# Performance work log

Hardware: AMD Instinct MI355X
Metric: run time of the kernel (lower is better)

The kernel has to match this reference:

```python
import jax, jax.numpy as jnp
import numpy as np

NUM_PERTS = 20000
D = 256          # embedding_dim
B, C = 64, 512   # batch_size, num_cells
EPS = 1e-5


def setup_inputs() -> dict:
    key = jax.random.key(0)
    ks = jax.random.split(key, 20)
    inp = {
        'perturbation_ids': jax.random.randint(ks[0], (B, C), 0, NUM_PERTS),
        'table': jax.random.normal(ks[1], (NUM_PERTS, D), dtype=jnp.float32),
    }
    s = 1.0 / np.sqrt(D)
    for i in range(4):
        inp[f'W{i+1}'] = jax.random.uniform(ks[2 + 2 * i], (D, D), minval=-s, maxval=s, dtype=jnp.float32)
        inp[f'b{i+1}'] = jax.random.uniform(ks[3 + 2 * i], (D,), minval=-s, maxval=s, dtype=jnp.float32)
    for i in range(3):
        inp[f'g{i+1}'] = jnp.ones((D,), jnp.float32)
        inp[f'be{i+1}'] = jnp.zeros((D,), jnp.float32)
    return inp


def _bn(x, gamma, beta):
    # BatchNorm1d forward with batch statistics (training-mode math, biased var)
    mu = jnp.mean(x, axis=0)
    var = jnp.mean(jnp.square(x - mu), axis=0)
    return (x - mu) * jax.lax.rsqrt(var + EPS) * gamma + beta


def reference(perturbation_ids, table,
              W1, b1, W2, b2, W3, b3, W4, b4,
              g1, be1, g2, be2, g3, be3):
    # Vectorized replacement of the Python double-loop dict gather
    emb = table[perturbation_ids]                 # (B, C, D)
    x = emb.reshape(-1, D)                        # (B*C, D)
    x = _bn(jax.nn.gelu(x @ W1 + b1, approximate=False), g1, be1)
    x = _bn(jax.nn.gelu(x @ W2 + b2, approximate=False), g2, be2)
    x = _bn(jax.nn.gelu(x @ W3 + b3, approximate=False), g3, be3)
    x = jax.nn.gelu(x @ W4 + b4, approximate=False)
    return x.reshape(B, C, D)
```

## Files before the change

### kernel.cpp

```cpp
#include <hip/hip_runtime.h>
#include <math.h>


typedef __attribute__((ext_vector_type(8))) short short8;
typedef __attribute__((ext_vector_type(4))) float floatx4;

#define DDIM 256

__device__ __forceinline__ unsigned short f2bf(float f) {
    union { float f; unsigned int u; } v; v.f = f;
    unsigned int r = v.u + 0x7fffu + ((v.u >> 16) & 1u);
    return (unsigned short)(r >> 16);
}
__device__ __forceinline__ float bf2f(unsigned short u) {
    union { unsigned int i; float f; } v; v.i = ((unsigned int)u) << 16;
    return v.f;
}
__device__ __forceinline__ float gelu_fast(float x) {
    float z = 0.7978845608f * (x + 0.044715f * x * x * x);
    float e = __expf(2.0f * z);
    float th = 1.0f - 2.0f * __builtin_amdgcn_rcpf(1.0f + e);
    return 0.5f * x * (1.0f + th);
}

__global__ void prep_kernel(const float* __restrict__ W0,
                            const float* __restrict__ W1,
                            const float* __restrict__ W2,
                            const float* __restrict__ W3,
                            unsigned short* __restrict__ Wt ,
                            float* __restrict__ stats )
{
    const int t = threadIdx.x, b = blockIdx.x;
    const int j = b >> 8, n = b & 255;
    const float* W = (j == 0) ? W0 : (j == 1) ? W1 : (j == 2) ? W2 : W3;
    Wt[((size_t)j << 16) + (size_t)t * DDIM + n] = f2bf(W[(size_t)n * DDIM + t]);
    if (b < 12) {
        float* s = stats + b * 1024;
        s[t] = 0.f; s[t + 256] = 0.f; s[t + 512] = 0.f; s[t + 768] = 0.f;
    }
}

template<int GATHER, int AFFINE, int WRITE_F32, int DO_STATS>
__global__ __launch_bounds__(256, 4)
void gemm_enc(const unsigned short* __restrict__ A,
              const int* __restrict__ ids,
              const float* __restrict__ table,
              const unsigned short* __restrict__ Wt,
              const float* __restrict__ bias,
              const float* __restrict__ statsIn,
              const float* __restrict__ gma,
              const float* __restrict__ bta,
              void* __restrict__ outp,
              float* __restrict__ statShards)
{
    __shared__ alignas(16) unsigned short Albs[32 * 256];
    __shared__ float sc[256], sh[256];

    const int tid  = threadIdx.x;
    const int blk  = blockIdx.x;
    const int wave = tid >> 6;
    const int lane = tid & 63;
    const int quad = lane >> 4;
    const int l15  = lane & 15;
    const int wn   = wave;
    const int row0 = blk * 32;

    if (AFFINE) {
        float sum = 0.f, sq = 0.f;
#pragma unroll
        for (int s = 0; s < 8; ++s) {
            sum += statsIn[s * 512 + tid];
            sq  += statsIn[s * 512 + 256 + tid];
        }
        const float mu  = sum * (1.f / 32768.f);
        const float var = sq * (1.f / 32768.f) - mu * mu;
        const float scl = rsqrtf(var + 1e-5f) * gma[tid];
        sc[tid] = scl;
        sh[tid] = bta[tid] - mu * scl;
        __syncthreads();
    }

    {
        const int r  = tid & 31;
        const int ci = tid >> 5;
        const int c0 = ci * 32;
        if (GATHER) {
            const int src = ids[row0 + r];
            const float* tp = table + (size_t)src * DDIM + c0;
#pragma unroll
            for (int j = 0; j < 4; ++j) {
                float4 v0 = *(const float4*)(tp + j * 8);
                float4 v1 = *(const float4*)(tp + j * 8 + 4);
                union { unsigned short u[8]; uint4 v; } o;
                o.u[0]=f2bf(v0.x); o.u[1]=f2bf(v0.y); o.u[2]=f2bf(v0.z); o.u[3]=f2bf(v0.w);
                o.u[4]=f2bf(v1.x); o.u[5]=f2bf(v1.y); o.u[6]=f2bf(v1.z); o.u[7]=f2bf(v1.w);
                const int g = ci * 4 + j;
                *(uint4*)(Albs + r * 256 + (g ^ (r & 7)) * 8) = o.v;
            }
        } else {
            const unsigned short* ap = A + (size_t)(row0 + r) * DDIM + c0;
#pragma unroll
            for (int j = 0; j < 4; ++j) {
                union { unsigned short u[8]; uint4 v; } o;
                o.v = *(const uint4*)(ap + j * 8);
                if (AFFINE) {
#pragma unroll
                    for (int e = 0; e < 8; ++e) {
                        const int c = c0 + j * 8 + e;
                        o.u[e] = f2bf(fmaf(bf2f(o.u[e]), sc[c], sh[c]));
                    }
                }
                const int g = ci * 4 + j;
                *(uint4*)(Albs + r * 256 + (g ^ (r & 7)) * 8) = o.v;
            }
        }
    }

    float bias_v[4];
#pragma unroll
    for (int nt = 0; nt < 4; ++nt)
        bias_v[nt] = bias[wn * 64 + nt * 16 + l15];

    floatx4 acc[2][4];
#pragma unroll
    for (int i = 0; i < 2; ++i)
#pragma unroll
        for (int j = 0; j < 4; ++j)
            acc[i][j] = floatx4{0.f, 0.f, 0.f, 0.f};

    __syncthreads();

    const unsigned short* wb = Wt + (size_t)(wn * 64 + l15) * DDIM + quad * 8;
#pragma unroll 2
    for (int kk = 0; kk < 8; ++kk) {
        short8 bfr[4];
#pragma unroll
        for (int nt = 0; nt < 4; ++nt)
            bfr[nt] = *(const short8*)(wb + (size_t)(nt * 16) * DDIM + kk * 32);
        short8 af[2];
        const int agp = ((kk * 4 + quad) ^ (l15 & 7)) * 8;
#pragma unroll
        for (int mt = 0; mt < 2; ++mt)
            af[mt] = *(const short8*)(Albs + (mt * 16 + l15) * 256 + agp);
#pragma unroll
        for (int mt = 0; mt < 2; ++mt)
#pragma unroll
            for (int nt = 0; nt < 4; ++nt)
                acc[mt][nt] = __builtin_amdgcn_mfma_f32_16x16x32_bf16(
                    af[mt], bfr[nt], acc[mt][nt], 0, 0, 0);
    }

    float s1[4] = {0.f, 0.f, 0.f, 0.f};
    float s2[4] = {0.f, 0.f, 0.f, 0.f};
#pragma unroll
    for (int mt = 0; mt < 2; ++mt) {
        const int rb = row0 + mt * 16 + quad * 4;
#pragma unroll
        for (int nt = 0; nt < 4; ++nt) {
            const int col = wn * 64 + nt * 16 + l15;
#pragma unroll
            for (int i = 0; i < 4; ++i) {
                float y = gelu_fast(acc[mt][nt][i] + bias_v[nt]);
                if (WRITE_F32) {
                    ((float*)outp)[(size_t)(rb + i) * DDIM + col] = y;
                } else {
                    ((unsigned short*)outp)[(size_t)(rb + i) * DDIM + col] = f2bf(y);
                }
                if (DO_STATS) { s1[nt] += y; s2[nt] += y * y; }
            }
        }
    }
    if (DO_STATS) {
#pragma unroll
        for (int nt = 0; nt < 4; ++nt) {
            s1[nt] += __shfl_xor(s1[nt], 16); s1[nt] += __shfl_xor(s1[nt], 32);
            s2[nt] += __shfl_xor(s2[nt], 16); s2[nt] += __shfl_xor(s2[nt], 32);
        }
        float* sb = statShards + (blk & 7) * 512;
        if (quad == 0) {
#pragma unroll
            for (int nt = 0; nt < 4; ++nt) {
                const int col = wn * 64 + nt * 16 + l15;
                atomicAdd(&sb[col],       s1[nt]);
                atomicAdd(&sb[256 + col], s2[nt]);
            }
        }
    }
}

extern "C" void kernel_launch(void* const* d_in, const int* in_sizes, int n_in,
                              void* d_out, int out_size, void* d_ws, size_t ws_size,
                              hipStream_t stream)
{
    const int*   ids   = (const int*)  d_in[0];
    const float* table = (const float*)d_in[1];
    const float* W1 = (const float*)d_in[2];  const float* b1 = (const float*)d_in[3];
    const float* W2 = (const float*)d_in[4];  const float* b2 = (const float*)d_in[5];
    const float* W3 = (const float*)d_in[6];  const float* b3 = (const float*)d_in[7];
    const float* W4 = (const float*)d_in[8];  const float* b4 = (const float*)d_in[9];
    const float* g1 = (const float*)d_in[10]; const float* be1 = (const float*)d_in[11];
    const float* g2 = (const float*)d_in[12]; const float* be2 = (const float*)d_in[13];
    const float* g3 = (const float*)d_in[14]; const float* be3 = (const float*)d_in[15];

    unsigned char* ws = (unsigned char*)d_ws;
    unsigned short* Wt   = (unsigned short*)ws;
    float* stats = (float*)(ws + (size_t)524288);
    unsigned short* act1 = (unsigned short*)(ws + (size_t)1048576);
    unsigned short* act2 = (unsigned short*)(ws + (size_t)17825792);
    unsigned short* Wt1 = Wt;
    unsigned short* Wt2 = Wt + 65536;
    unsigned short* Wt3 = Wt + 131072;
    unsigned short* Wt4 = Wt + 196608;

    prep_kernel<<<1024, 256, 0, stream>>>(W1, W2, W3, W4, Wt, stats);

    gemm_enc<1, 0, 0, 1><<<1024, 256, 0, stream>>>(
        nullptr, ids, table, Wt1, b1, nullptr, nullptr, nullptr, act1, stats);
    gemm_enc<0, 1, 0, 1><<<1024, 256, 0, stream>>>(
        act1, nullptr, nullptr, Wt2, b2, stats, g1, be1, act2, stats + 4096);
    gemm_enc<0, 1, 0, 1><<<1024, 256, 0, stream>>>(
        act2, nullptr, nullptr, Wt3, b3, stats + 4096, g2, be2, act1, stats + 8192);
    gemm_enc<0, 1, 1, 0><<<1024, 256, 0, stream>>>(
        act1, nullptr, nullptr, Wt4, b4, stats + 8192, g3, be3, (void*)d_out, nullptr);
}
```

Before: 199.1 us.

## Double row tile to 64 per block and software-pipeline MFMA operand loads

Each block now processes 64 rows instead of 32, so each wave computes a 4x4 grid of MFMA tiles and reuses each loaded weight fragment across twice as many rows. The grid is halved to 512 blocks and launch bounds lowered to 2 blocks per SM to allow more registers. The k-loop is fully unrolled with register double-buffering, so the next step's A and B fragments are loaded while the current MFMAs run. This trades occupancy and grid parallelism for fewer weight loads and better hiding of load latency.

```diff
diff --git a/kernel.cpp b/kernel.cpp
--- a/kernel.cpp
+++ b/kernel.cpp
@@ -41,7 +41,7 @@
 }
 
 template<int GATHER, int AFFINE, int WRITE_F32, int DO_STATS>
-__global__ __launch_bounds__(256, 4)
+__global__ __launch_bounds__(256, 2)
 void gemm_enc(const unsigned short* __restrict__ A,
               const int* __restrict__ ids,
               const float* __restrict__ table,
@@ -53,7 +53,7 @@
               void* __restrict__ outp,
               float* __restrict__ statShards)
 {
-    __shared__ alignas(16) unsigned short Albs[32 * 256];
+    __shared__ alignas(16) unsigned short Albs[64 * 256];
     __shared__ float sc[256], sh[256];
 
     const int tid  = threadIdx.x;
@@ -63,7 +63,7 @@
     const int quad = lane >> 4;
     const int l15  = lane & 15;
     const int wn   = wave;
-    const int row0 = blk * 32;
+    const int row0 = blk * 64;
 
     if (AFFINE) {
         float sum = 0.f, sq = 0.f;
@@ -81,26 +81,25 @@
     }
 
     {
-        const int r  = tid & 31;
-        const int ci = tid >> 5;
-        const int c0 = ci * 32;
+        const int r  = tid >> 2;
+        const int c0 = (tid & 3) * 64;
         if (GATHER) {
             const int src = ids[row0 + r];
             const float* tp = table + (size_t)src * DDIM + c0;
 #pragma unroll
-            for (int j = 0; j < 4; ++j) {
+            for (int j = 0; j < 8; ++j) {
                 float4 v0 = *(const float4*)(tp + j * 8);
                 float4 v1 = *(const float4*)(tp + j * 8 + 4);
                 union { unsigned short u[8]; uint4 v; } o;
                 o.u[0]=f2bf(v0.x); o.u[1]=f2bf(v0.y); o.u[2]=f2bf(v0.z); o.u[3]=f2bf(v0.w);
                 o.u[4]=f2bf(v1.x); o.u[5]=f2bf(v1.y); o.u[6]=f2bf(v1.z); o.u[7]=f2bf(v1.w);
-                const int g = ci * 4 + j;
+                const int g = (tid & 3) * 8 + j;
                 *(uint4*)(Albs + r * 256 + (g ^ (r & 7)) * 8) = o.v;
             }
         } else {
             const unsigned short* ap = A + (size_t)(row0 + r) * DDIM + c0;
 #pragma unroll
-            for (int j = 0; j < 4; ++j) {
+            for (int j = 0; j < 8; ++j) {
                 union { unsigned short u[8]; uint4 v; } o;
                 o.v = *(const uint4*)(ap + j * 8);
                 if (AFFINE) {
@@ -110,7 +109,7 @@
                         o.u[e] = f2bf(fmaf(bf2f(o.u[e]), sc[c], sh[c]));
                     }
                 }
-                const int g = ci * 4 + j;
+                const int g = (tid & 3) * 8 + j;
                 *(uint4*)(Albs + r * 256 + (g ^ (r & 7)) * 8) = o.v;
             }
         }
@@ -121,9 +120,9 @@
     for (int nt = 0; nt < 4; ++nt)
         bias_v[nt] = bias[wn * 64 + nt * 16 + l15];
 
-    floatx4 acc[2][4];
-#pragma unroll
-    for (int i = 0; i < 2; ++i)
+    floatx4 acc[4][4];
+#pragma unroll
+    for (int i = 0; i < 4; ++i)
 #pragma unroll
         for (int j = 0; j < 4; ++j)
             acc[i][j] = floatx4{0.f, 0.f, 0.f, 0.f};
@@ -131,29 +130,42 @@
     __syncthreads();
 
     const unsigned short* wb = Wt + (size_t)(wn * 64 + l15) * DDIM + quad * 8;
-#pragma unroll 2
+    short8 bfr[4], bnx[4], af[4], anx[4];
+    {
+        const int agp = (quad ^ (l15 & 7)) * 8;
+#pragma unroll
+        for (int nt = 0; nt < 4; ++nt)
+            bfr[nt] = *(const short8*)(wb + (size_t)(nt * 16) * DDIM);
+#pragma unroll
+        for (int mt = 0; mt < 4; ++mt)
+            af[mt] = *(const short8*)(Albs + (mt * 16 + l15) * 256 + agp);
+    }
+#pragma unroll
     for (int kk = 0; kk < 8; ++kk) {
-        short8 bfr[4];
-#pragma unroll
-        for (int nt = 0; nt < 4; ++nt)
-            bfr[nt] = *(const short8*)(wb + (size_t)(nt * 16) * DDIM + kk * 32);
-        short8 af[2];
-        const int agp = ((kk * 4 + quad) ^ (l15 & 7)) * 8;
-#pragma unroll
-        for (int mt = 0; mt < 2; ++mt)
-            af[mt] = *(const short8*)(Albs + (mt * 16 + l15) * 256 + agp);
-#pragma unroll
-        for (int mt = 0; mt < 2; ++mt)
+        if (kk < 7) {
+            const int agp = (((kk + 1) * 4 + quad) ^ (l15 & 7)) * 8;
+#pragma unroll
+            for (int nt = 0; nt < 4; ++nt)
+                bnx[nt] = *(const short8*)(wb + (size_t)(nt * 16) * DDIM
+                                           + (kk + 1) * 32);
+#pragma unroll
+            for (int mt = 0; mt < 4; ++mt)
+                anx[mt] = *(const short8*)(Albs + (mt * 16 + l15) * 256 + agp);
+        }
+#pragma unroll
+        for (int mt = 0; mt < 4; ++mt)
 #pragma unroll
             for (int nt = 0; nt < 4; ++nt)
                 acc[mt][nt] = __builtin_amdgcn_mfma_f32_16x16x32_bf16(
                     af[mt], bfr[nt], acc[mt][nt], 0, 0, 0);
+#pragma unroll
+        for (int x = 0; x < 4; ++x) { af[x] = anx[x]; bfr[x] = bnx[x]; }
     }
 
     float s1[4] = {0.f, 0.f, 0.f, 0.f};
     float s2[4] = {0.f, 0.f, 0.f, 0.f};
 #pragma unroll
-    for (int mt = 0; mt < 2; ++mt) {
+    for (int mt = 0; mt < 4; ++mt) {
         const int rb = row0 + mt * 16 + quad * 4;
 #pragma unroll
         for (int nt = 0; nt < 4; ++nt) {
@@ -214,12 +226,12 @@
 
     prep_kernel<<<1024, 256, 0, stream>>>(W1, W2, W3, W4, Wt, stats);
 
-    gemm_enc<1, 0, 0, 1><<<1024, 256, 0, stream>>>(
+    gemm_enc<1, 0, 0, 1><<<512, 256, 0, stream>>>(
         nullptr, ids, table, Wt1, b1, nullptr, nullptr, nullptr, act1, stats);
-    gemm_enc<0, 1, 0, 1><<<1024, 256, 0, stream>>>(
+    gemm_enc<0, 1, 0, 1><<<512, 256, 0, stream>>>(
         act1, nullptr, nullptr, Wt2, b2, stats, g1, be1, act2, stats + 4096);
-    gemm_enc<0, 1, 0, 1><<<1024, 256, 0, stream>>>(
+    gemm_enc<0, 1, 0, 1><<<512, 256, 0, stream>>>(
         act2, nullptr, nullptr, Wt3, b3, stats + 4096, g2, be2, act1, stats + 8192);
-    gemm_enc<0, 1, 1, 0><<<1024, 256, 0, stream>>>(
+    gemm_enc<0, 1, 1, 0><<<512, 256, 0, stream>>>(
         act1, nullptr, nullptr, Wt4, b4, stats + 8192, g3, be3, (void*)d_out, nullptr);
 }
```

Result: faster. 181.7 us (-8.8%).
